# Kernel optimization log

Measured on AMD Instinct MI355X. Metric: run time of the kernel, lower is better.

The kernel has to match this reference:

```python
import jax, jax.numpy as jnp
import numpy as np

EMBED_DIM = 1024
N_HEADS = 16
HEAD_DIM = EMBED_DIM // N_HEADS


def setup_inputs() -> dict:
    key = jax.random.key(0)
    k_x, k_qw, k_qb, k_ow, k_ob = jax.random.split(key, 5)
    s = 1.0 / np.sqrt(EMBED_DIM)
    return {
        "x": jax.random.normal(k_x, (2, 2048, EMBED_DIM), dtype=jnp.float32),
        "qkv_w": jax.random.uniform(k_qw, (3 * EMBED_DIM, EMBED_DIM), jnp.float32, -s, s),
        "qkv_b": jax.random.uniform(k_qb, (3 * EMBED_DIM,), jnp.float32, -s, s),
        "out_w": jax.random.uniform(k_ow, (EMBED_DIM, EMBED_DIM), jnp.float32, -s, s),
        "out_b": jax.random.uniform(k_ob, (EMBED_DIM,), jnp.float32, -s, s),
    }


def reference(x, qkv_w, qkv_b, out_w, out_b):
    B, S, E = x.shape
    # fused QKV projection (torch Linear: x @ W^T + b)
    qkv = x @ qkv_w.T + qkv_b                      # [B,S,3E]
    qkv = qkv.reshape(B, S, N_HEADS, 3 * HEAD_DIM).transpose(0, 2, 1, 3)  # [B,H,S,3d]
    q, k, v = jnp.split(qkv, 3, axis=-1)           # each [B,H,S,d]
    scores = jnp.einsum("bhqd,bhkd->bhqk", q, k) / jnp.sqrt(jnp.float32(HEAD_DIM))
    weights = jax.nn.softmax(scores, axis=-1)      # [B,H,S,S]
    attn = jnp.einsum("bhqk,bhkd->bhqd", weights, v)
    attn = attn.transpose(0, 2, 1, 3).reshape(B, S, E)
    return attn @ out_w.T + out_b
```

## Files before the change

### kernel.cpp

```cpp
#include <hip/hip_runtime.h>
#include <hip/hip_bf16.h>


#define E_DIM   1024
#define NHEADS  16
#define HDIM    64
#define SEQ     2048
#define TOK     4096
#define QKV_DIM 3072
#define QK_STRIDE 2048
#define QSCALE_F 0.18033688011112042f

typedef __attribute__((ext_vector_type(8))) short bf16x8;
typedef __attribute__((ext_vector_type(4))) float f32x4;
typedef __attribute__((ext_vector_type(4))) int   i32x4;
typedef __attribute__((ext_vector_type(2))) int   i32x2;
typedef __attribute__((ext_vector_type(2))) __bf16 bf16x2_t;

#if __has_builtin(__builtin_amdgcn_exp2f)
#define EXP2F(x) __builtin_amdgcn_exp2f(x)
#else
#define EXP2F(x) exp2f(x)
#endif

__device__ __forceinline__ unsigned pack2bf(float a, float b) {
#if __has_builtin(__builtin_amdgcn_cvt_pk_bf16_f32)
    union { bf16x2_t v; unsigned u; } u;
    u.v = __builtin_amdgcn_cvt_pk_bf16_f32(a, b);
    return u.u;
#else
    union { float f; unsigned u; } ua, ub; ua.f = a; ub.f = b;
    unsigned ra = ua.u + 0x7FFF + ((ua.u >> 16) & 1);
    unsigned rb = ub.u + 0x7FFF + ((ub.u >> 16) & 1);
    return (ra >> 16) | (rb & 0xFFFF0000u);
#endif
}

__device__ __forceinline__ unsigned short f2bf(float x) {
    return (unsigned short)(pack2bf(x, x) & 0xFFFFu);
}

__device__ __forceinline__ void load_lds16(const void* g, void* l) {
    __builtin_amdgcn_global_load_lds(
        (const __attribute__((address_space(1))) void*)g,
        (__attribute__((address_space(3))) void*)l, 16, 0, 0);
}

__device__ __forceinline__ bf16x8 lds_read8(const unsigned short* p) {
    union { i32x4 i; bf16x8 b; } u;
    u.i = *(const i32x4*)p;
    return u.b;
}

__device__ __forceinline__ f32x4 mfma16(bf16x8 a, bf16x8 b, f32x4 c) {
    return __builtin_amdgcn_mfma_f32_16x16x32_bf16(a, b, c, 0, 0, 0);
}

__global__ void cast3_kernel(const float* __restrict__ a, unsigned short* __restrict__ oa, int na4,
                             const float* __restrict__ b, unsigned short* __restrict__ ob, int nb4,
                             const float* __restrict__ c, unsigned short* __restrict__ oc) {
    int i = blockIdx.x * blockDim.x + threadIdx.x;
    const float* src; unsigned short* dst; int j;
    if (i < na4)            { src = a; dst = oa; j = i; }
    else if (i < na4 + nb4) { src = b; dst = ob; j = i - na4; }
    else                    { src = c; dst = oc; j = i - na4 - nb4; }
    f32x4 v = ((const f32x4*)src)[j];
    union { i32x2 i2; unsigned u[2]; } o;
    o.u[0] = pack2bf(v.x, v.y);
    o.u[1] = pack2bf(v.z, v.w);
    ((i32x2*)dst)[j] = o.i2;
}

__global__ __launch_bounds__(256, 3)
void gemm_qkv_kernel(const unsigned short* __restrict__ A,
                     const unsigned short* __restrict__ B,
                     const float* __restrict__ bias,
                     unsigned short* __restrict__ qk,
                     unsigned short* __restrict__ vT,
                     int K) {
    __shared__ __align__(16) unsigned short As[128 * 64];
    __shared__ __align__(16) unsigned short Bs[128 * 64];

    const int tid  = threadIdx.x;
    const int wave = tid >> 6, lane = tid & 63;
    const int quad = lane >> 4, l16 = lane & 15;
    const int row0 = blockIdx.y * 128, col0 = blockIdx.x * 128;
    const int wr = (wave >> 1) * 64, wc = (wave & 1) * 64;

    f32x4 acc[4][4];
#pragma unroll
    for (int i = 0; i < 4; ++i)
#pragma unroll
        for (int j = 0; j < 4; ++j) acc[i][j] = (f32x4){0.f, 0.f, 0.f, 0.f};

    const int nkt = K >> 6;
    for (int kt = 0; kt < nkt; ++kt) {
        const int k0 = kt << 6;
#pragma unroll
        for (int i = 0; i < 4; ++i) {
            int p = i * 256 + tid;
            int r = p >> 3;
            int kc = (p & 7) ^ (r & 7);
            load_lds16(A + (size_t)(row0 + r) * K + k0 + kc * 8, &As[p * 8]);
        }
#pragma unroll
        for (int i = 0; i < 4; ++i) {
            int p = i * 256 + tid;
            int r = p >> 3;
            int kc = (p & 7) ^ (r & 7);
            load_lds16(B + (size_t)(col0 + r) * K + k0 + kc * 8, &Bs[p * 8]);
        }
        __syncthreads();

#pragma unroll
        for (int ks = 0; ks < 2; ++ks) {
            bf16x8 af[4], bfr[4];
#pragma unroll
            for (int rb = 0; rb < 4; ++rb) {
                int r_l  = wr + rb * 16 + l16;
                int phys = (ks * 4 + quad) ^ (l16 & 7);
                af[rb] = lds_read8(&As[r_l * 64 + phys * 8]);
            }
#pragma unroll
            for (int cb = 0; cb < 4; ++cb) {
                int r_l  = wc + cb * 16 + l16;
                int phys = (ks * 4 + quad) ^ (l16 & 7);
                bfr[cb] = lds_read8(&Bs[r_l * 64 + phys * 8]);
            }
#pragma unroll
            for (int rb = 0; rb < 4; ++rb)
#pragma unroll
                for (int cb = 0; cb < 4; ++cb)
                    acc[rb][cb] = mfma16(af[rb], bfr[cb], acc[rb][cb]);
        }
        __syncthreads();
    }

#pragma unroll
    for (int rb = 0; rb < 4; ++rb)
#pragma unroll
        for (int cb = 0; cb < 4; ++cb) {
            int col = col0 + wc + cb * 16 + l16;
            int h    = col / 192;
            int part = col - h * 192;
            float bv = bias[col];
            int row_b = row0 + wr + rb * 16 + quad * 4;
            float v[4];
#pragma unroll
            for (int reg = 0; reg < 4; ++reg) v[reg] = acc[rb][cb][reg] + bv;
            if (part < 128) {
                float sc = (part < 64) ? QSCALE_F : 1.0f;
                size_t base = (size_t)h * 128 + part;
#pragma unroll
                for (int reg = 0; reg < 4; ++reg)
                    qk[(size_t)(row_b + reg) * QK_STRIDE + base] = f2bf(v[reg] * sc);
            } else {
                int i  = part - 128;
                int b  = row_b >> 11;
                int s  = row_b & 2047;
                i32x2 pk;
                pk.x = (int)pack2bf(v[0], v[1]);
                pk.y = (int)pack2bf(v[2], v[3]);
                *(i32x2*)&vT[(((size_t)(b * 16 + h)) * 64 + i) * SEQ + s] = pk;
            }
        }
}

__global__ __launch_bounds__(256, 2)
void gemm2_kernel(const unsigned short* __restrict__ A,
                  const unsigned short* __restrict__ B,
                  const float* __restrict__ bias,
                  float* __restrict__ C, int M, int N, int K) {
    __shared__ __align__(16) unsigned short As[128 * 64];
    __shared__ __align__(16) unsigned short Bs[64 * 64];

    const int tid  = threadIdx.x;
    const int wave = tid >> 6, lane = tid & 63;
    const int quad = lane >> 4, l16 = lane & 15;
    const int row0 = blockIdx.y * 128, col0 = blockIdx.x * 64;
    const int wr = wave * 32;

    f32x4 acc[2][4];
#pragma unroll
    for (int i = 0; i < 2; ++i)
#pragma unroll
        for (int j = 0; j < 4; ++j) acc[i][j] = (f32x4){0.f, 0.f, 0.f, 0.f};

    const int nkt = K >> 6;
    for (int kt = 0; kt < nkt; ++kt) {
        const int k0 = kt << 6;
#pragma unroll
        for (int i = 0; i < 4; ++i) {
            int p = i * 256 + tid;
            int r = p >> 3;
            int kc = (p & 7) ^ (r & 7);
            load_lds16(A + (size_t)(row0 + r) * K + k0 + kc * 8, &As[p * 8]);
        }
#pragma unroll
        for (int i = 0; i < 2; ++i) {
            int p = i * 256 + tid;
            int r = p >> 3;
            int kc = (p & 7) ^ (r & 7);
            load_lds16(B + (size_t)(col0 + r) * K + k0 + kc * 8, &Bs[p * 8]);
        }
        __syncthreads();

#pragma unroll
        for (int ks = 0; ks < 2; ++ks) {
            bf16x8 af[2], bfr[4];
#pragma unroll
            for (int rb = 0; rb < 2; ++rb) {
                int r_l  = wr + rb * 16 + l16;
                int phys = (ks * 4 + quad) ^ (l16 & 7);
                af[rb] = lds_read8(&As[r_l * 64 + phys * 8]);
            }
#pragma unroll
            for (int cb = 0; cb < 4; ++cb) {
                int r_l  = cb * 16 + l16;
                int phys = (ks * 4 + quad) ^ (l16 & 7);
                bfr[cb] = lds_read8(&Bs[r_l * 64 + phys * 8]);
            }
#pragma unroll
            for (int rb = 0; rb < 2; ++rb)
#pragma unroll
                for (int cb = 0; cb < 4; ++cb)
                    acc[rb][cb] = mfma16(af[rb], bfr[cb], acc[rb][cb]);
        }
        __syncthreads();
    }

#pragma unroll
    for (int rb = 0; rb < 2; ++rb)
#pragma unroll
        for (int cb = 0; cb < 4; ++cb) {
            int col = col0 + cb * 16 + l16;
            float bv = bias[col];
#pragma unroll
            for (int reg = 0; reg < 4; ++reg) {
                int row = row0 + wr + rb * 16 + quad * 4 + reg;
                C[(size_t)row * N + col] = acc[rb][cb][reg] + bv;
            }
        }
}

__global__ __launch_bounds__(512, 4)
void attn_kernel(const unsigned short* __restrict__ qk,
                 const unsigned short* __restrict__ vT,
                 unsigned short* __restrict__ attn) {
    __shared__ __align__(16) unsigned short Ks[128 * 64];
    __shared__ __align__(16) unsigned short Vs[64 * 128];
    __shared__ __align__(16) unsigned short Ps[8][16 * 64];

    const int tid  = threadIdx.x;
    const int wave = tid >> 6, lane = tid & 63;
    const int quad = lane >> 4, l16 = lane & 15;
    const int bh = blockIdx.y;
    const int b = bh >> 4, h = bh & 15;
    const int q0 = blockIdx.x * 128;
    const size_t rowbase = (size_t)b * SEQ;
    const int qtok = q0 + wave * 16 + l16;

    const int sw3 = l16 & 7;
    const unsigned short* Kb0 = &Ks[l16 * 64 + ((quad ^ sw3) * 8)];
    const unsigned short* Kb1 = &Ks[l16 * 64 + (((4 + quad) ^ sw3) * 8)];
    const unsigned short* Vb[4] = {
        &Vs[l16 * 128 + (((0 * 4 + quad) ^ l16) * 8)],
        &Vs[l16 * 128 + (((1 * 4 + quad) ^ l16) * 8)],
        &Vs[l16 * 128 + (((2 * 4 + quad) ^ l16) * 8)],
        &Vs[l16 * 128 + (((3 * 4 + quad) ^ l16) * 8)] };
    unsigned short* Pw[4];
#pragma unroll
    for (int c4 = 0; c4 < 4; ++c4)
        Pw[c4] = &Ps[wave][l16 * 64 + (((c4 * 2 + (quad >> 1)) ^ sw3) * 8) + (quad & 1) * 4];
    const unsigned short* Pr0 = &Ps[wave][l16 * 64 + ((quad ^ sw3) * 8)];
    const unsigned short* Pr1 = &Ps[wave][l16 * 64 + (((4 + quad) ^ sw3) * 8)];

    bf16x8 qf[2];
#pragma unroll
    for (int ks = 0; ks < 2; ++ks) {
        const unsigned short* p =
            qk + (rowbase + qtok) * QK_STRIDE + h * 128 + ks * 32 + quad * 8;
        union { i32x4 i; bf16x8 b; } u;
        u.i = *(const i32x4*)p;
        qf[ks] = u.b;
    }

    f32x4 o[4];
#pragma unroll
    for (int ib = 0; ib < 4; ++ib) o[ib] = (f32x4){0.f, 0.f, 0.f, 0.f};
    float l_s = 0.f;

    for (int kt = 0; kt < SEQ / 128; ++kt) {
        const int kb = kt * 128;
        const unsigned short* kbase = qk + (rowbase + kb) * QK_STRIDE + h * 128 + 64;
        const unsigned short* vbase = vT + (size_t)bh * 64 * SEQ + kb;
#pragma unroll
        for (int i = 0; i < 2; ++i) {
            int p = i * 512 + tid;
            int r = p >> 3;
            int kc = (p & 7) ^ (r & 7);
            load_lds16(kbase + r * QK_STRIDE + kc * 8, &Ks[p * 8]);
        }
#pragma unroll
        for (int i = 0; i < 2; ++i) {
            int p = i * 512 + tid;
            int r = p >> 4;
            int c = (p & 15) ^ (r & 15);
            load_lds16(vbase + r * SEQ + c * 8, &Vs[p * 8]);
        }
        __syncthreads();

        f32x4 s[8];
#pragma unroll
        for (int cb = 0; cb < 8; ++cb) s[cb] = (f32x4){0.f, 0.f, 0.f, 0.f};
#pragma unroll
        for (int cb = 0; cb < 8; ++cb) {
            bf16x8 kf0 = lds_read8(Kb0 + cb * 1024);
            s[cb] = mfma16(kf0, qf[0], s[cb]);
        }
#pragma unroll
        for (int cb = 0; cb < 8; ++cb) {
            bf16x8 kf1 = lds_read8(Kb1 + cb * 1024);
            s[cb] = mfma16(kf1, qf[1], s[cb]);
        }

        float rs = 0.f;
#pragma unroll
        for (int cb = 0; cb < 8; ++cb)
#pragma unroll
            for (int r = 0; r < 4; ++r) {
                float pv = EXP2F(s[cb][r]);
                s[cb][r] = pv;
                rs += pv;
            }
        rs += __shfl_xor(rs, 16);
        rs += __shfl_xor(rs, 32);
        l_s += rs;

#pragma unroll
        for (int half = 0; half < 2; ++half) {
#pragma unroll
            for (int c4 = 0; c4 < 4; ++c4) {
                int cb = half * 4 + c4;
                i32x2 pk;
                pk.x = (int)pack2bf(s[cb][0], s[cb][1]);
                pk.y = (int)pack2bf(s[cb][2], s[cb][3]);
                *(i32x2*)Pw[c4] = pk;
            }
            __asm__ volatile("s_waitcnt lgkmcnt(0)" ::: "memory");
            {
                bf16x8 pf0 = lds_read8(Pr0);
#pragma unroll
                for (int ib = 0; ib < 4; ++ib) {
                    bf16x8 vf = lds_read8(Vb[half * 2 + 0] + ib * 2048);
                    o[ib] = mfma16(pf0, vf, o[ib]);
                }
                bf16x8 pf1 = lds_read8(Pr1);
#pragma unroll
                for (int ib = 0; ib < 4; ++ib) {
                    bf16x8 vf = lds_read8(Vb[half * 2 + 1] + ib * 2048);
                    o[ib] = mfma16(pf1, vf, o[ib]);
                }
            }
        }
        __syncthreads();
    }

    float il[4];
#pragma unroll
    for (int r = 0; r < 4; ++r) il[r] = 1.0f / __shfl(l_s, quad * 4 + r);
#pragma unroll
    for (int ib = 0; ib < 4; ++ib)
#pragma unroll
        for (int r = 0; r < 4; ++r) {
            int t = q0 + wave * 16 + quad * 4 + r;
            attn[(rowbase + t) * E_DIM + h * 64 + ib * 16 + l16] =
                f2bf(o[ib][r] * il[r]);
        }
}

extern "C" void kernel_launch(void* const* d_in, const int* in_sizes, int n_in,
                              void* d_out, int out_size, void* d_ws, size_t ws_size,
                              hipStream_t stream) {
    const float* x     = (const float*)d_in[0];
    const float* qkv_w = (const float*)d_in[1];
    const float* qkv_b = (const float*)d_in[2];
    const float* out_w = (const float*)d_in[3];
    const float* out_b = (const float*)d_in[4];

    char* ws = (char*)d_ws;
    unsigned short* xb   = (unsigned short*)(ws);
    unsigned short* wqkv = (unsigned short*)(ws + 8388608);
    unsigned short* wout = (unsigned short*)(ws + 14680064);
    unsigned short* qk   = (unsigned short*)(ws + 16777216);
    unsigned short* attn = (unsigned short*)(ws + 33554432);
    unsigned short* vT   = (unsigned short*)(ws + 41943040);

    cast3_kernel<<<8192, 256, 0, stream>>>(x, xb, 1048576,
                                           qkv_w, wqkv, 786432,
                                           out_w, wout);

    gemm_qkv_kernel<<<dim3(24, 32), 256, 0, stream>>>(
        xb, wqkv, qkv_b, qk, vT, E_DIM);

    attn_kernel<<<dim3(16, 32), 512, 0, stream>>>(qk, vT, attn);

    gemm2_kernel<<<dim3(16, 32), 256, 0, stream>>>(
        attn, wout, out_b, (float*)d_out, TOK, E_DIM, E_DIM);
}
```

Before: 182.4 us.

## Double-buffer K/V tiles in attention and raise MFMA wave priority

The attention kernel now uses two LDS buffers for K and V. The next tile's global-to-LDS loads are issued before the current tile is computed, with vmcnt waits and raw barriers in place of the full __syncthreads. This aims to hide global load latency behind the QK^T, exp and PV work. It also brackets MFMA sections with s_setprio to favour matrix issue, at the cost of double the K/V LDS footprint, which may reduce occupancy.

Result: no change. 183.6 us (+0.6%).

```diff
diff --git a/kernel.cpp b/kernel.cpp
--- a/kernel.cpp
+++ b/kernel.cpp
@@ -243,12 +243,80 @@
         }
 }
 
+
+#define STAGE(BUF, KT) do {                                                    \
+    const unsigned short* kbase_ =                                             \
+        qk + (rowbase + (KT) * 128) * QK_STRIDE + h * 128 + 64;                \
+    const unsigned short* vbase_ = vT + (size_t)bh * 64 * SEQ + (KT) * 128;    \
+    _Pragma("unroll") for (int i_ = 0; i_ < 2; ++i_) {                         \
+        int p_ = i_ * 512 + tid; int r_ = p_ >> 3;                             \
+        int kc_ = (p_ & 7) ^ (r_ & 7);                                         \
+        load_lds16(kbase_ + r_ * QK_STRIDE + kc_ * 8, &Ks[BUF][p_ * 8]);       \
+    }                                                                          \
+    _Pragma("unroll") for (int i_ = 0; i_ < 2; ++i_) {                         \
+        int p_ = i_ * 512 + tid; int r_ = p_ >> 4;                             \
+        int c_ = (p_ & 15) ^ (r_ & 15);                                        \
+        load_lds16(vbase_ + r_ * SEQ + c_ * 8, &Vs[BUF][p_ * 8]);              \
+    }                                                                          \
+} while (0)
+
+#define COMPUTE_TILE(BUF) do {                                                 \
+    constexpr int KO_ = (BUF) * 8192;         \
+    f32x4 s[8];                                                                \
+    _Pragma("unroll") for (int cb = 0; cb < 8; ++cb)                           \
+        s[cb] = (f32x4){0.f, 0.f, 0.f, 0.f};                                   \
+    __builtin_amdgcn_s_setprio(1);                                             \
+    _Pragma("unroll") for (int cb = 0; cb < 8; ++cb) {                         \
+        bf16x8 kf0 = lds_read8(Kb0 + KO_ + cb * 1024);                         \
+        s[cb] = mfma16(kf0, qf[0], s[cb]);                                     \
+    }                                                                          \
+    _Pragma("unroll") for (int cb = 0; cb < 8; ++cb) {                         \
+        bf16x8 kf1 = lds_read8(Kb1 + KO_ + cb * 1024);                         \
+        s[cb] = mfma16(kf1, qf[1], s[cb]);                                     \
+    }                                                                          \
+    __builtin_amdgcn_s_setprio(0);                                             \
+    float rs = 0.f;                                                            \
+    _Pragma("unroll") for (int cb = 0; cb < 8; ++cb)                           \
+        _Pragma("unroll") for (int r = 0; r < 4; ++r) {                        \
+            float pv = EXP2F(s[cb][r]);                                        \
+            s[cb][r] = pv;                                                     \
+            rs += pv;                                                          \
+        }                                                                      \
+    rs += __shfl_xor(rs, 16);                                                  \
+    rs += __shfl_xor(rs, 32);                                                  \
+    l_s += rs;                                                                 \
+    _Pragma("unroll") for (int half = 0; half < 2; ++half) {                   \
+        _Pragma("unroll") for (int c4 = 0; c4 < 4; ++c4) {                     \
+            int cb = half * 4 + c4;                                            \
+            i32x2 pk;                                                          \
+            pk.x = (int)pack2bf(s[cb][0], s[cb][1]);                           \
+            pk.y = (int)pack2bf(s[cb][2], s[cb][3]);                           \
+            *(i32x2*)Pw[c4] = pk;                                              \
+        }                                                                      \
+        __asm__ volatile("s_waitcnt lgkmcnt(0)" ::: "memory");                 \
+        __builtin_amdgcn_s_setprio(1);                                         \
+        {                                                                      \
+            bf16x8 pf0 = lds_read8(Pr0);                                       \
+            _Pragma("unroll") for (int ib = 0; ib < 4; ++ib) {                 \
+                bf16x8 vf = lds_read8(Vb[half * 2 + 0] + KO_ + ib * 2048);     \
+                o[ib] = mfma16(pf0, vf, o[ib]);                                \
+            }                                                                  \
+            bf16x8 pf1 = lds_read8(Pr1);                                       \
+            _Pragma("unroll") for (int ib = 0; ib < 4; ++ib) {                 \
+                bf16x8 vf = lds_read8(Vb[half * 2 + 1] + KO_ + ib * 2048);     \
+                o[ib] = mfma16(pf1, vf, o[ib]);                                \
+            }                                                                  \
+        }                                                                      \
+        __builtin_amdgcn_s_setprio(0);                                         \
+    }                                                                          \
+} while (0)
+
 __global__ __launch_bounds__(512, 4)
 void attn_kernel(const unsigned short* __restrict__ qk,
                  const unsigned short* __restrict__ vT,
                  unsigned short* __restrict__ attn) {
-    __shared__ __align__(16) unsigned short Ks[128 * 64];
-    __shared__ __align__(16) unsigned short Vs[64 * 128];
+    __shared__ __align__(16) unsigned short Ks[2][128 * 64];
+    __shared__ __align__(16) unsigned short Vs[2][64 * 128];
     __shared__ __align__(16) unsigned short Ps[8][16 * 64];
 
     const int tid  = threadIdx.x;
@@ -261,13 +329,13 @@
     const int qtok = q0 + wave * 16 + l16;
 
     const int sw3 = l16 & 7;
-    const unsigned short* Kb0 = &Ks[l16 * 64 + ((quad ^ sw3) * 8)];
-    const unsigned short* Kb1 = &Ks[l16 * 64 + (((4 + quad) ^ sw3) * 8)];
+    const unsigned short* Kb0 = &Ks[0][l16 * 64 + ((quad ^ sw3) * 8)];
+    const unsigned short* Kb1 = &Ks[0][l16 * 64 + (((4 + quad) ^ sw3) * 8)];
     const unsigned short* Vb[4] = {
-        &Vs[l16 * 128 + (((0 * 4 + quad) ^ l16) * 8)],
-        &Vs[l16 * 128 + (((1 * 4 + quad) ^ l16) * 8)],
-        &Vs[l16 * 128 + (((2 * 4 + quad) ^ l16) * 8)],
-        &Vs[l16 * 128 + (((3 * 4 + quad) ^ l16) * 8)] };
+        &Vs[0][l16 * 128 + (((0 * 4 + quad) ^ l16) * 8)],
+        &Vs[0][l16 * 128 + (((1 * 4 + quad) ^ l16) * 8)],
+        &Vs[0][l16 * 128 + (((2 * 4 + quad) ^ l16) * 8)],
+        &Vs[0][l16 * 128 + (((3 * 4 + quad) ^ l16) * 8)] };
     unsigned short* Pw[4];
 #pragma unroll
     for (int c4 = 0; c4 < 4; ++c4)
@@ -290,80 +358,23 @@
     for (int ib = 0; ib < 4; ++ib) o[ib] = (f32x4){0.f, 0.f, 0.f, 0.f};
     float l_s = 0.f;
 
-    for (int kt = 0; kt < SEQ / 128; ++kt) {
-        const int kb = kt * 128;
-        const unsigned short* kbase = qk + (rowbase + kb) * QK_STRIDE + h * 128 + 64;
-        const unsigned short* vbase = vT + (size_t)bh * 64 * SEQ + kb;
-#pragma unroll
-        for (int i = 0; i < 2; ++i) {
-            int p = i * 512 + tid;
-            int r = p >> 3;
-            int kc = (p & 7) ^ (r & 7);
-            load_lds16(kbase + r * QK_STRIDE + kc * 8, &Ks[p * 8]);
-        }
-#pragma unroll
-        for (int i = 0; i < 2; ++i) {
-            int p = i * 512 + tid;
-            int r = p >> 4;
-            int c = (p & 15) ^ (r & 15);
-            load_lds16(vbase + r * SEQ + c * 8, &Vs[p * 8]);
-        }
-        __syncthreads();
-
-        f32x4 s[8];
-#pragma unroll
-        for (int cb = 0; cb < 8; ++cb) s[cb] = (f32x4){0.f, 0.f, 0.f, 0.f};
-#pragma unroll
-        for (int cb = 0; cb < 8; ++cb) {
-            bf16x8 kf0 = lds_read8(Kb0 + cb * 1024);
-            s[cb] = mfma16(kf0, qf[0], s[cb]);
-        }
-#pragma unroll
-        for (int cb = 0; cb < 8; ++cb) {
-            bf16x8 kf1 = lds_read8(Kb1 + cb * 1024);
-            s[cb] = mfma16(kf1, qf[1], s[cb]);
-        }
-
-        float rs = 0.f;
-#pragma unroll
-        for (int cb = 0; cb < 8; ++cb)
-#pragma unroll
-            for (int r = 0; r < 4; ++r) {
-                float pv = EXP2F(s[cb][r]);
-                s[cb][r] = pv;
-                rs += pv;
-            }
-        rs += __shfl_xor(rs, 16);
-        rs += __shfl_xor(rs, 32);
-        l_s += rs;
-
-#pragma unroll
-        for (int half = 0; half < 2; ++half) {
-#pragma unroll
-            for (int c4 = 0; c4 < 4; ++c4) {
-                int cb = half * 4 + c4;
-                i32x2 pk;
-                pk.x = (int)pack2bf(s[cb][0], s[cb][1]);
-                pk.y = (int)pack2bf(s[cb][2], s[cb][3]);
-                *(i32x2*)Pw[c4] = pk;
-            }
-            __asm__ volatile("s_waitcnt lgkmcnt(0)" ::: "memory");
-            {
-                bf16x8 pf0 = lds_read8(Pr0);
-#pragma unroll
-                for (int ib = 0; ib < 4; ++ib) {
-                    bf16x8 vf = lds_read8(Vb[half * 2 + 0] + ib * 2048);
-                    o[ib] = mfma16(pf0, vf, o[ib]);
-                }
-                bf16x8 pf1 = lds_read8(Pr1);
-#pragma unroll
-                for (int ib = 0; ib < 4; ++ib) {
-                    bf16x8 vf = lds_read8(Vb[half * 2 + 1] + ib * 2048);
-                    o[ib] = mfma16(pf1, vf, o[ib]);
-                }
-            }
-        }
-        __syncthreads();
+    STAGE(0, 0);
+#pragma unroll 1
+    for (int kt = 0; kt < SEQ / 128; kt += 2) {
+        STAGE(1, kt + 1);
+        __asm__ volatile("s_waitcnt vmcnt(4)" ::: "memory");
+        __builtin_amdgcn_s_barrier();
+        COMPUTE_TILE(0);
+        __builtin_amdgcn_s_barrier();
+        if (kt + 2 < SEQ / 128) {
+            STAGE(0, kt + 2);
+            __asm__ volatile("s_waitcnt vmcnt(4)" ::: "memory");
+        } else {
+            __asm__ volatile("s_waitcnt vmcnt(0)" ::: "memory");
+        }
+        __builtin_amdgcn_s_barrier();
+        COMPUTE_TILE(1);
+        __builtin_amdgcn_s_barrier();
     }
 
     float il[4];
```

## Swizzle attention block order, widen P buffer, add setprio around MFMA phases

Applied to the files above, without the earlier changes.

Remaps the flat block index so that consecutive workgroups are spread across different (batch, head) pairs, which is intended to improve L2/cache locality across the chip. P tiles are now written all at once into a doubled per-wave LDS buffer, so there is a single wait followed by one PV loop instead of two half passes. Global and LDS load pointers are precomputed and advanced by increment, the exp row sum becomes a tree reduction, and s_setprio is raised around the MFMA sections so waves in their matrix phase get issue priority. The cost is more LDS per block, which may reduce occupancy.

New measurement: 184.8 us. No clear change (+1.3%).

```diff
diff --git a/kernel.cpp b/kernel.cpp
--- a/kernel.cpp
+++ b/kernel.cpp
@@ -249,14 +249,17 @@
                  unsigned short* __restrict__ attn) {
     __shared__ __align__(16) unsigned short Ks[128 * 64];
     __shared__ __align__(16) unsigned short Vs[64 * 128];
-    __shared__ __align__(16) unsigned short Ps[8][16 * 64];
+    __shared__ __align__(16) unsigned short Ps[8][16 * 128];
 
     const int tid  = threadIdx.x;
     const int wave = tid >> 6, lane = tid & 63;
     const int quad = lane >> 4, l16 = lane & 15;
-    const int bh = blockIdx.y;
+
+    const int flat = blockIdx.y * 16 + blockIdx.x;
+    const int swz  = (flat & 7) * 64 + (flat >> 3);
+    const int bh = swz >> 4;
     const int b = bh >> 4, h = bh & 15;
-    const int q0 = blockIdx.x * 128;
+    const int q0 = (swz & 15) * 128;
     const size_t rowbase = (size_t)b * SEQ;
     const int qtok = q0 + wave * 16 + l16;
 
@@ -268,12 +271,27 @@
         &Vs[l16 * 128 + (((1 * 4 + quad) ^ l16) * 8)],
         &Vs[l16 * 128 + (((2 * 4 + quad) ^ l16) * 8)],
         &Vs[l16 * 128 + (((3 * 4 + quad) ^ l16) * 8)] };
-    unsigned short* Pw[4];
-#pragma unroll
-    for (int c4 = 0; c4 < 4; ++c4)
-        Pw[c4] = &Ps[wave][l16 * 64 + (((c4 * 2 + (quad >> 1)) ^ sw3) * 8) + (quad & 1) * 4];
-    const unsigned short* Pr0 = &Ps[wave][l16 * 64 + ((quad ^ sw3) * 8)];
-    const unsigned short* Pr1 = &Ps[wave][l16 * 64 + (((4 + quad) ^ sw3) * 8)];
+    unsigned short* Pw[8];
+#pragma unroll
+    for (int cb = 0; cb < 8; ++cb)
+        Pw[cb] = &Ps[wave][l16 * 128 + (((cb * 2 + (quad >> 1)) ^ sw3) * 8) + (quad & 1) * 4];
+    const unsigned short* Pr[4];
+#pragma unroll
+    for (int ks2 = 0; ks2 < 4; ++ks2)
+        Pr[ks2] = &Ps[wave][l16 * 128 + (((ks2 * 4 + quad) ^ sw3) * 8)];
+
+    const unsigned short* kg[2]; unsigned short* lk[2];
+    const unsigned short* vg[2]; unsigned short* lv[2];
+#pragma unroll
+    for (int i = 0; i < 2; ++i) {
+        int p = i * 512 + tid;
+        { int r = p >> 3; int kc = (p & 7) ^ (r & 7);
+          kg[i] = qk + (rowbase) * QK_STRIDE + h * 128 + 64 + (size_t)r * QK_STRIDE + kc * 8;
+          lk[i] = &Ks[p * 8]; }
+        { int r = p >> 4; int c = (p & 15) ^ (r & 15);
+          vg[i] = vT + (size_t)bh * 64 * SEQ + (size_t)r * SEQ + c * 8;
+          lv[i] = &Vs[p * 8]; }
+    }
 
     bf16x8 qf[2];
 #pragma unroll
@@ -291,28 +309,19 @@
     float l_s = 0.f;
 
     for (int kt = 0; kt < SEQ / 128; ++kt) {
-        const int kb = kt * 128;
-        const unsigned short* kbase = qk + (rowbase + kb) * QK_STRIDE + h * 128 + 64;
-        const unsigned short* vbase = vT + (size_t)bh * 64 * SEQ + kb;
 #pragma unroll
         for (int i = 0; i < 2; ++i) {
-            int p = i * 512 + tid;
-            int r = p >> 3;
-            int kc = (p & 7) ^ (r & 7);
-            load_lds16(kbase + r * QK_STRIDE + kc * 8, &Ks[p * 8]);
-        }
-#pragma unroll
-        for (int i = 0; i < 2; ++i) {
-            int p = i * 512 + tid;
-            int r = p >> 4;
-            int c = (p & 15) ^ (r & 15);
-            load_lds16(vbase + r * SEQ + c * 8, &Vs[p * 8]);
+            load_lds16(kg[i], lk[i]);
+            load_lds16(vg[i], lv[i]);
+            kg[i] += 128 * QK_STRIDE;
+            vg[i] += 128;
         }
         __syncthreads();
 
         f32x4 s[8];
 #pragma unroll
         for (int cb = 0; cb < 8; ++cb) s[cb] = (f32x4){0.f, 0.f, 0.f, 0.f};
+        __builtin_amdgcn_s_setprio(1);
 #pragma unroll
         for (int cb = 0; cb < 8; ++cb) {
             bf16x8 kf0 = lds_read8(Kb0 + cb * 1024);
@@ -323,46 +332,41 @@
             bf16x8 kf1 = lds_read8(Kb1 + cb * 1024);
             s[cb] = mfma16(kf1, qf[1], s[cb]);
         }
-
-        float rs = 0.f;
+        __builtin_amdgcn_s_setprio(0);
+
 #pragma unroll
         for (int cb = 0; cb < 8; ++cb)
 #pragma unroll
-            for (int r = 0; r < 4; ++r) {
-                float pv = EXP2F(s[cb][r]);
-                s[cb][r] = pv;
-                rs += pv;
-            }
-        rs += __shfl_xor(rs, 16);
-        rs += __shfl_xor(rs, 32);
-        l_s += rs;
-
-#pragma unroll
-        for (int half = 0; half < 2; ++half) {
-#pragma unroll
-            for (int c4 = 0; c4 < 4; ++c4) {
-                int cb = half * 4 + c4;
-                i32x2 pk;
-                pk.x = (int)pack2bf(s[cb][0], s[cb][1]);
-                pk.y = (int)pack2bf(s[cb][2], s[cb][3]);
-                *(i32x2*)Pw[c4] = pk;
-            }
-            __asm__ volatile("s_waitcnt lgkmcnt(0)" ::: "memory");
-            {
-                bf16x8 pf0 = lds_read8(Pr0);
-#pragma unroll
-                for (int ib = 0; ib < 4; ++ib) {
-                    bf16x8 vf = lds_read8(Vb[half * 2 + 0] + ib * 2048);
-                    o[ib] = mfma16(pf0, vf, o[ib]);
-                }
-                bf16x8 pf1 = lds_read8(Pr1);
-#pragma unroll
-                for (int ib = 0; ib < 4; ++ib) {
-                    bf16x8 vf = lds_read8(Vb[half * 2 + 1] + ib * 2048);
-                    o[ib] = mfma16(pf1, vf, o[ib]);
-                }
-            }
-        }
+            for (int r = 0; r < 4; ++r) s[cb][r] = EXP2F(s[cb][r]);
+        {
+            f32x4 t0 = s[0] + s[1], t1 = s[2] + s[3];
+            f32x4 t2 = s[4] + s[5], t3 = s[6] + s[7];
+            t0 += t1; t2 += t3; t0 += t2;
+            float rs = (t0[0] + t0[1]) + (t0[2] + t0[3]);
+            rs += __shfl_xor(rs, 16);
+            rs += __shfl_xor(rs, 32);
+            l_s += rs;
+        }
+
+#pragma unroll
+        for (int cb = 0; cb < 8; ++cb) {
+            i32x2 pk;
+            pk.x = (int)pack2bf(s[cb][0], s[cb][1]);
+            pk.y = (int)pack2bf(s[cb][2], s[cb][3]);
+            *(i32x2*)Pw[cb] = pk;
+        }
+        __asm__ volatile("s_waitcnt lgkmcnt(0)" ::: "memory");
+        __builtin_amdgcn_s_setprio(1);
+#pragma unroll
+        for (int ks2 = 0; ks2 < 4; ++ks2) {
+            bf16x8 pf = lds_read8(Pr[ks2]);
+#pragma unroll
+            for (int ib = 0; ib < 4; ++ib) {
+                bf16x8 vf = lds_read8(Vb[ks2] + ib * 2048);
+                o[ib] = mfma16(pf, vf, o[ib]);
+            }
+        }
+        __builtin_amdgcn_s_setprio(0);
         __syncthreads();
     }
 
```

## Halve attention block size, swizzle block order, precompute load pointers, add setprio

Applied to the files above, without the earlier changes.

The attention kernel now runs 4 waves per block over 64 query rows instead of 8 waves over 128, with twice as many blocks. A block-index swizzle spreads consecutive blocks across different heads, which changes L2 reuse and how work is balanced across CUs. K/V global load pointers are precomputed and bumped each tile to remove address math, MFMA sections are wrapped in s_setprio, and the row-sum reduction becomes a vector tree. Smaller blocks reload each K/V tile once per 64 queries instead of per 128, which doubles LDS fill traffic relative to compute.

After: 187.1 us. 1.03x slower.

```diff
diff --git a/kernel.cpp b/kernel.cpp
--- a/kernel.cpp
+++ b/kernel.cpp
@@ -243,20 +243,23 @@
         }
 }
 
-__global__ __launch_bounds__(512, 4)
+__global__ __launch_bounds__(256, 4)
 void attn_kernel(const unsigned short* __restrict__ qk,
                  const unsigned short* __restrict__ vT,
                  unsigned short* __restrict__ attn) {
     __shared__ __align__(16) unsigned short Ks[128 * 64];
     __shared__ __align__(16) unsigned short Vs[64 * 128];
-    __shared__ __align__(16) unsigned short Ps[8][16 * 64];
+    __shared__ __align__(16) unsigned short Ps[4][16 * 64];
 
     const int tid  = threadIdx.x;
     const int wave = tid >> 6, lane = tid & 63;
     const int quad = lane >> 4, l16 = lane & 15;
-    const int bh = blockIdx.y;
+
+    const int flat = blockIdx.y * 32 + blockIdx.x;
+    const int swz  = (flat & 7) * 128 + (flat >> 3);
+    const int bh = swz >> 5;
     const int b = bh >> 4, h = bh & 15;
-    const int q0 = blockIdx.x * 128;
+    const int q0 = (swz & 31) * 64;
     const size_t rowbase = (size_t)b * SEQ;
     const int qtok = q0 + wave * 16 + l16;
 
@@ -275,6 +278,19 @@
     const unsigned short* Pr0 = &Ps[wave][l16 * 64 + ((quad ^ sw3) * 8)];
     const unsigned short* Pr1 = &Ps[wave][l16 * 64 + (((4 + quad) ^ sw3) * 8)];
 
+    const unsigned short* kg[4]; unsigned short* lk[4];
+    const unsigned short* vg[4]; unsigned short* lv[4];
+#pragma unroll
+    for (int i = 0; i < 4; ++i) {
+        int p = i * 256 + tid;
+        { int r = p >> 3; int kc = (p & 7) ^ (r & 7);
+          kg[i] = qk + rowbase * QK_STRIDE + h * 128 + 64 + (size_t)r * QK_STRIDE + kc * 8;
+          lk[i] = &Ks[p * 8]; }
+        { int r = p >> 4; int c = (p & 15) ^ (r & 15);
+          vg[i] = vT + (size_t)bh * 64 * SEQ + (size_t)r * SEQ + c * 8;
+          lv[i] = &Vs[p * 8]; }
+    }
+
     bf16x8 qf[2];
 #pragma unroll
     for (int ks = 0; ks < 2; ++ks) {
@@ -291,28 +307,19 @@
     float l_s = 0.f;
 
     for (int kt = 0; kt < SEQ / 128; ++kt) {
-        const int kb = kt * 128;
-        const unsigned short* kbase = qk + (rowbase + kb) * QK_STRIDE + h * 128 + 64;
-        const unsigned short* vbase = vT + (size_t)bh * 64 * SEQ + kb;
-#pragma unroll
-        for (int i = 0; i < 2; ++i) {
-            int p = i * 512 + tid;
-            int r = p >> 3;
-            int kc = (p & 7) ^ (r & 7);
-            load_lds16(kbase + r * QK_STRIDE + kc * 8, &Ks[p * 8]);
-        }
-#pragma unroll
-        for (int i = 0; i < 2; ++i) {
-            int p = i * 512 + tid;
-            int r = p >> 4;
-            int c = (p & 15) ^ (r & 15);
-            load_lds16(vbase + r * SEQ + c * 8, &Vs[p * 8]);
+#pragma unroll
+        for (int i = 0; i < 4; ++i) {
+            load_lds16(kg[i], lk[i]);
+            load_lds16(vg[i], lv[i]);
+            kg[i] += 128 * QK_STRIDE;
+            vg[i] += 128;
         }
         __syncthreads();
 
         f32x4 s[8];
 #pragma unroll
         for (int cb = 0; cb < 8; ++cb) s[cb] = (f32x4){0.f, 0.f, 0.f, 0.f};
+        __builtin_amdgcn_s_setprio(1);
 #pragma unroll
         for (int cb = 0; cb < 8; ++cb) {
             bf16x8 kf0 = lds_read8(Kb0 + cb * 1024);
@@ -323,19 +330,21 @@
             bf16x8 kf1 = lds_read8(Kb1 + cb * 1024);
             s[cb] = mfma16(kf1, qf[1], s[cb]);
         }
-
-        float rs = 0.f;
+        __builtin_amdgcn_s_setprio(0);
+
 #pragma unroll
         for (int cb = 0; cb < 8; ++cb)
 #pragma unroll
-            for (int r = 0; r < 4; ++r) {
-                float pv = EXP2F(s[cb][r]);
-                s[cb][r] = pv;
-                rs += pv;
-            }
-        rs += __shfl_xor(rs, 16);
-        rs += __shfl_xor(rs, 32);
-        l_s += rs;
+            for (int r = 0; r < 4; ++r) s[cb][r] = EXP2F(s[cb][r]);
+        {
+            f32x4 t0 = s[0] + s[1], t1 = s[2] + s[3];
+            f32x4 t2 = s[4] + s[5], t3 = s[6] + s[7];
+            t0 += t1; t2 += t3; t0 += t2;
+            float rs = (t0[0] + t0[1]) + (t0[2] + t0[3]);
+            rs += __shfl_xor(rs, 16);
+            rs += __shfl_xor(rs, 32);
+            l_s += rs;
+        }
 
 #pragma unroll
         for (int half = 0; half < 2; ++half) {
@@ -348,6 +357,7 @@
                 *(i32x2*)Pw[c4] = pk;
             }
             __asm__ volatile("s_waitcnt lgkmcnt(0)" ::: "memory");
+            __builtin_amdgcn_s_setprio(1);
             {
                 bf16x8 pf0 = lds_read8(Pr0);
 #pragma unroll
@@ -362,6 +372,7 @@
                     o[ib] = mfma16(pf1, vf, o[ib]);
                 }
             }
+            __builtin_amdgcn_s_setprio(0);
         }
         __syncthreads();
     }
@@ -403,7 +414,7 @@
     gemm_qkv_kernel<<<dim3(24, 32), 256, 0, stream>>>(
         xb, wqkv, qkv_b, qk, vT, E_DIM);
 
-    attn_kernel<<<dim3(16, 32), 512, 0, stream>>>(qk, vT, attn);
+    attn_kernel<<<dim3(32, 32), 256, 0, stream>>>(qk, vT, attn);
 
     gemm2_kernel<<<dim3(16, 32), 256, 0, stream>>>(
         attn, wout, out_b, (float*)d_out, TOK, E_DIM, E_DIM);
```
